# Kernel tuning notes

Measured on AMD Instinct MI355X. Metric: run time of the kernel, lower is better.

Reference implementation:

```python
import jax, jax.numpy as jnp
import numpy as np

DT = 0.001
TAU_MEM = 0.02
TAU_SYN = 0.005
THRESHOLD = 1.0


def conv2d(x, w, b, stride, pad):
    # x: [N,C,H,W], w: [O,I,kh,kw]
    y = jax.lax.conv_general_dilated(
        x, w, window_strides=(stride, stride),
        padding=[(pad, pad), (pad, pad)],
        dimension_numbers=("NCHW", "OIHW", "NCHW"))
    return y + b[None, :, None, None]


def lif_scan(current_t_first):
    # current_t_first: [T, B, C, H, W]; LIF with reset='subtract'
    alpha = jnp.exp(jnp.asarray(-DT / TAU_MEM, dtype=current_t_first.dtype))
    beta = jnp.exp(jnp.asarray(-DT / TAU_SYN, dtype=current_t_first.dtype))
    state_shape = current_t_first.shape[1:]
    init = (jnp.zeros(state_shape, current_t_first.dtype),
            jnp.zeros(state_shape, current_t_first.dtype))

    def step(carry, i_t):
        syn, mem = carry
        syn = beta * syn + i_t
        mem = alpha * mem + syn
        spike = (mem >= THRESHOLD).astype(i_t.dtype)
        mem = mem - THRESHOLD * spike  # subtract reset
        return (syn, mem), spike

    _, spikes = jax.lax.scan(step, init, current_t_first)
    return spikes  # [T, B, C, H, W]


def spiking_conv(x, w, b, stride, pad):
    # x: [B, C, H, W, T] -> spikes [B, O, H', W', T]
    B, C, H, W, T = x.shape
    xt = jnp.moveaxis(x, -1, 0)                 # [T,B,C,H,W]
    y = conv2d(xt.reshape(T * B, C, H, W), w, b, stride, pad)
    y = y.reshape(T, B, *y.shape[1:])           # [T,B,O,H',W']
    spikes = lif_scan(y)
    return jnp.moveaxis(spikes, 0, -1)          # [B,O,H',W',T]


def setup_inputs() -> dict:
    key = jax.random.key(0)
    ks = jax.random.split(key, 9)
    B, H, W, T = 4, 128, 128, 10
    num_classes = 80
    det_ch = (num_classes + 5) * 3  # 255

    def init_w(k, shape):
        fan_in = shape[1] * shape[2] * shape[3]
        bound = 1.0 / np.sqrt(fan_in)
        return jax.random.uniform(k, shape, jnp.float32, -bound, bound)

    x = jax.random.uniform(ks[0], (B, 2, H, W, T), jnp.float32)
    return {
        "x": x,
        "w1": init_w(ks[1], (64, 2, 3, 3)),   "b1": jax.random.uniform(ks[2], (64,), jnp.float32, -0.2, 0.2),
        "w2": init_w(ks[3], (128, 64, 3, 3)), "b2": jax.random.uniform(ks[4], (128,), jnp.float32, -0.04, 0.04),
        "w3": init_w(ks[5], (256, 128, 3, 3)),"b3": jax.random.uniform(ks[6], (256,), jnp.float32, -0.03, 0.03),
        "wd": init_w(ks[7], (det_ch, 256, 1, 1)), "bd": jax.random.uniform(ks[8], (det_ch,), jnp.float32, -0.06, 0.06),
    }


def reference(x, w1, b1, w2, b2, w3, b3, wd, bd):
    h = spiking_conv(x, w1, b1, stride=1, pad=1)   # [B,64,128,128,T]
    h = spiking_conv(h, w2, b2, stride=2, pad=1)   # [B,128,64,64,T]
    h = spiking_conv(h, w3, b3, stride=2, pad=1)   # [B,256,32,32,T]
    h_pooled = jnp.mean(h, axis=-1)                # mean over time
    detections = conv2d(h_pooled, wd, bd, stride=1, pad=0)  # [B,255,32,32]
    return detections
```

## Files before the change

kernel.cpp:

```cpp
#include <hip/hip_runtime.h>
#include <stdint.h>
#include <string.h>
#include <cmath>


#define BB 4
#define TT 10

typedef short bf16x8 __attribute__((ext_vector_type(8)));
typedef float f32x4  __attribute__((ext_vector_type(4)));

#define MFMA16(a, b, c) __builtin_amdgcn_mfma_f32_16x16x32_bf16((a), (b), (c), 0, 0, 0)


__global__ __launch_bounds__(256) void zpad1v(uint32_t* __restrict__ buf) {
    uint32_t* p = buf + (size_t)blockIdx.x * 544896u;
    for (int i = threadIdx.x; i < 8320; i += 256) {
        if (i < 4224) p[i] = 0u;
        else {
            int j = i - 4224;
            int row = 1 + (j >> 5), cih = (j >> 4) & 1, e = j & 15;
            p[row * 4224 + 2112 + cih * 1056 + e] = 0u;
        }
    }
}

__global__ __launch_bounds__(256) void zpad3v(uint32_t* __restrict__ buf) {
    uint32_t* p = buf + (size_t)blockIdx.x * 282880u;
    for (int i = threadIdx.x; i < 8448; i += 256) {
        if (i < 4352) p[i] = 0u;
        else {
            int j = i - 4352;
            int row = 1 + (j >> 6), cih = (j >> 4) & 3, e = j & 15;
            p[row * 4352 + 2176 + cih * 544 + e] = 0u;
        }
    }
}

__global__ __launch_bounds__(256) void conv1_lif(
    const float* __restrict__ x,
    const float* __restrict__ w1,
    const float* __restrict__ b1,
    unsigned short* __restrict__ s1p2,
    float alpha, float beta)
{
    __shared__ float xs[2][3][10][10];
    __shared__ float wsh[18][64];
    __shared__ uint32_t spk[40][68];
    const int tid = threadIdx.x;
    const int b = blockIdx.z, h = blockIdx.y, w0 = blockIdx.x * 8;

    for (int i = tid; i < 1152; i += 256) {
        int co = i & 63, tap = i >> 6;
        wsh[tap][co] = w1[co * 18 + tap];
    }
    for (int i = tid; i < 600; i += 256) {
        int t = i % 10; int rest = i / 10;
        int wi = rest % 10; rest /= 10;
        int kh = rest % 3; int ci = rest / 3;
        int hh = h - 1 + kh, ww = w0 - 1 + wi;
        float v = 0.f;
        if (hh >= 0 && hh < 128 && ww >= 0 && ww < 128)
            v = x[(((b * 2 + ci) * 128 + hh) * 128 + ww) * 10 + t];
        xs[ci][kh][wi][t] = v;
    }
    __syncthreads();

    const int px  = tid & 7;
    const int cog = (tid >> 3) * 2;
    float acc[2][10];
#pragma unroll
    for (int c = 0; c < 2; ++c)
#pragma unroll
        for (int t = 0; t < 10; ++t) acc[c][t] = 0.f;

#pragma unroll
    for (int tap = 0; tap < 18; ++tap) {
        const int ci = tap / 9, kh = (tap % 9) / 3, kw = tap % 3;
        float2 wv = *(const float2*)&wsh[tap][cog];
#pragma unroll
        for (int t = 0; t < 10; ++t) {
            float xv = xs[ci][kh][px + kw][t];
            acc[0][t] = __fmaf_rn(wv.x, xv, acc[0][t]);
            acc[1][t] = __fmaf_rn(wv.y, xv, acc[1][t]);
        }
    }
    const int pr    = px & 1;
    const int col2l = px >> 1;
    const int comb0 = pr * 2 + (cog >> 5);
    const int ipos  = col2l * 16 + ((cog & 31) >> 1);
    const float bv0 = b1[cog], bv1 = b1[cog + 1];
    float syn0 = 0.f, mem0 = 0.f, syn1 = 0.f, mem1 = 0.f;
#pragma unroll
    for (int t = 0; t < 10; ++t) {
        float cur0 = __fadd_rn(acc[0][t], bv0);
        syn0 = __fadd_rn(__fmul_rn(beta, syn0), cur0);
        mem0 = __fadd_rn(__fmul_rn(alpha, mem0), syn0);
        bool s0 = (mem0 >= 1.0f);
        mem0 = __fsub_rn(mem0, s0 ? 1.0f : 0.0f);
        float cur1 = __fadd_rn(acc[1][t], bv1);
        syn1 = __fadd_rn(__fmul_rn(beta, syn1), cur1);
        mem1 = __fadd_rn(__fmul_rn(alpha, mem1), syn1);
        bool s1 = (mem1 >= 1.0f);
        mem1 = __fsub_rn(mem1, s1 ? 1.0f : 0.0f);
        spk[t * 4 + comb0][ipos] =
            (s0 ? 0x3F80u : 0u) | ((s1 ? 0x3F80u : 0u) << 16);
    }
    __syncthreads();

    uint32_t* sg = (uint32_t*)s1p2;
    const int e = tid & 63;
#pragma unroll
    for (int k = 0; k < 10; ++k) {
        const int combo = k * 4 + (tid >> 6);
        const int t  = combo >> 2;
        const int pp = (combo >> 1) & 1;
        const int ch = combo & 1;
        const uint32_t ga = (uint32_t)(t * BB + b) * 544896u
            + ((uint32_t)((h + 1) * 8448 + pp * 4224 + ch * 2112
                          + ((w0 >> 1) + pp) * 32) >> 1) + e;
        sg[ga] = spk[combo][e];
    }
}

__global__ __launch_bounds__(256) void wtrans2c(
    const float* __restrict__ w2, unsigned short* __restrict__ wtb)
{
    int i = blockIdx.x * 256 + threadIdx.x;
    if (i >= 73728) return;
    int co  = i / 576;
    int rem = i - co * 576;
    int ci  = rem / 9;
    int tap = rem - ci * 9;
    float w = w2[i];
    uint32_t uw  = __float_as_uint(w);
    uint32_t h16 = (uw + 0x7FFFu + ((uw >> 16) & 1u)) >> 16;
    float hf = __uint_as_float(h16 << 16);
    float r1 = w - hf;
    uint32_t ur1 = __float_as_uint(r1);
    uint32_t m16 = (ur1 + 0x7FFFu + ((ur1 >> 16) & 1u)) >> 16;
    float mf = __uint_as_float(m16 << 16);
    float r2 = r1 - mf;
    uint32_t ur2 = __float_as_uint(r2);
    uint32_t l16 = (ur2 + 0x7FFFu + ((ur2 >> 16) & 1u)) >> 16;

    int cobi = co >> 6, coL = co & 63;
    int wid = coL >> 4, l15 = coL & 15;
    int c = ci >> 5, r5 = ci & 31;
    int g = r5 >> 3, e = r5 & 7;
    size_t base = (size_t)(cobi * 27 + tap * 3) * 4096
                + (size_t)(((wid * 2 + c) * 64 + (g * 16 + l15)) * 8 + e);
    wtb[base]        = (unsigned short)h16;
    wtb[base + 4096] = (unsigned short)m16;
    wtb[base + 8192] = (unsigned short)l16;
}

__global__ __launch_bounds__(256) void wtrans3c(
    const float* __restrict__ w3, unsigned short* __restrict__ wtb)
{
    int i = blockIdx.x * 256 + threadIdx.x;
    if (i >= 294912) return;
    int co  = i / 1152;
    int rem = i - co * 1152;
    int ci  = rem / 9;
    int tap = rem - ci * 9;
    float w = w3[i];
    uint32_t uw  = __float_as_uint(w);
    uint32_t h16 = (uw + 0x7FFFu + ((uw >> 16) & 1u)) >> 16;
    float hf = __uint_as_float(h16 << 16);
    float r1 = w - hf;
    uint32_t ur1 = __float_as_uint(r1);
    uint32_t m16 = (ur1 + 0x7FFFu + ((ur1 >> 16) & 1u)) >> 16;
    float mf = __uint_as_float(m16 << 16);
    float r2 = r1 - mf;
    uint32_t ur2 = __float_as_uint(r2);
    uint32_t l16 = (ur2 + 0x7FFFu + ((ur2 >> 16) & 1u)) >> 16;

    int cobi = co >> 6, coL = co & 63;
    int wq = coL >> 4, l15 = coL & 15;
    int cc = ci >> 5, r5 = ci & 31;
    int g = r5 >> 3, e = r5 & 7;
    size_t base = (size_t)(cobi * 27 + tap * 3) * 8192
                + (size_t)(((wq * 4 + cc) * 64 + (g * 16 + l15)) * 8 + e);
    wtb[base]         = (unsigned short)h16;
    wtb[base + 8192]  = (unsigned short)m16;
    wtb[base + 16384] = (unsigned short)l16;
}

#define VMCNT(n) do { __builtin_amdgcn_sched_barrier(0); \
    asm volatile("s_waitcnt vmcnt(" #n ")" ::: "memory"); \
    __builtin_amdgcn_sched_barrier(0); } while (0)
#define SB() __builtin_amdgcn_sched_barrier(0)
#define BARR() do { __builtin_amdgcn_sched_barrier(0); \
    __builtin_amdgcn_s_barrier(); \
    __builtin_amdgcn_sched_barrier(0); } while (0)
#define PRIO1() __builtin_amdgcn_s_setprio(1)
#define PRIO0() __builtin_amdgcn_s_setprio(0)

__global__ __launch_bounds__(512) void conv2_mfma(
    const unsigned short* __restrict__ s1p2,
    const unsigned short* __restrict__ wtb,
    float* __restrict__ p2)
{
    __shared__ alignas(16) unsigned short Bs[3][4096];
    const int tid  = threadIdx.x;
    const int lane = tid & 63, w = tid >> 6;
    const int r = lane & 15, g = lane >> 4;
    const int f = blockIdx.z;
    const int hb = blockIdx.x;

    const unsigned short* fb = s1p2 + (uint32_t)f * 1089792u;
    const unsigned short* wB = wtb + (uint32_t)(w >> 2) * (27u * 4096u)
                             + (uint32_t)(w & 3) * 1024u + (uint32_t)lane * 8u;
    const uint32_t lfo = (uint32_t)(r * 32 + g * 8);

    f32x4 acc[4];
#pragma unroll
    for (int mt = 0; mt < 4; ++mt) acc[mt] = (f32x4){0.f, 0.f, 0.f, 0.f};
    bf16x8 bA[6], bB[6];

#define STAGE2(tap_, slot_) do { \
    const int kh_ = (tap_) / 3, kw_ = (tap_) % 3; \
    const int p_ = (kw_ == 1) ? 0 : 1; \
    const int cf_ = (kw_ == 2) ? 1 : 0; \
    const int mt_ = w >> 1, c_ = w & 1; \
    const unsigned short* src_ = fb + (uint32_t)(2 * hb + kh_) * 8448u \
        + (uint32_t)p_ * 4224u + (uint32_t)c_ * 2112u \
        + (uint32_t)(mt_ * 16 + cf_) * 32u + lfo; \
    __builtin_amdgcn_global_load_lds( \
        (const __attribute__((address_space(1))) unsigned int*)(const void*)src_, \
        (__attribute__((address_space(3))) unsigned int*)(void*)(&Bs[slot_][w * 512]), \
        16, 0, 0); \
} while (0)

#define LOADB2(tap_, DST) do { _Pragma("unroll") \
    for (int t_ = 0; t_ < 3; ++t_) { _Pragma("unroll") \
        for (int c_ = 0; c_ < 2; ++c_) \
            DST[t_ * 2 + c_] = *(const bf16x8*)(wB + (uint32_t)((tap_) * 3 + t_) * 4096u + c_ * 512u); \
    } } while (0)

#define COMP2(slot_, BU) do { \
    bf16x8 af_[8]; \
    _Pragma("unroll") \
    for (int q_ = 0; q_ < 8; ++q_) \
        af_[q_] = *(const bf16x8*)&Bs[slot_][q_ * 512 + lane * 8]; \
    _Pragma("unroll") \
    for (int t_ = 0; t_ < 3; ++t_) { _Pragma("unroll") \
        for (int c_ = 0; c_ < 2; ++c_) { \
            bf16x8 b_ = BU[t_ * 2 + c_]; \
            acc[0] = MFMA16(b_, af_[0 + c_], acc[0]); \
            acc[1] = MFMA16(b_, af_[2 + c_], acc[1]); \
            acc[2] = MFMA16(b_, af_[4 + c_], acc[2]); \
            acc[3] = MFMA16(b_, af_[6 + c_], acc[3]); \
        } } } while (0)

#define PH2(tap_, snxt_, scur_, BU, BN) do { \
    SB(); STAGE2((tap_) + 1, snxt_); LOADB2((tap_) + 1, BN); SB(); \
    VMCNT(7); BARR(); \
    PRIO1(); COMP2(scur_, BU); PRIO0(); SB(); \
} while (0)

    STAGE2(0, 0); LOADB2(0, bA);
    PH2(0, 1, 0, bA, bB); PH2(1, 2, 1, bB, bA); PH2(2, 0, 2, bA, bB);
    PH2(3, 1, 0, bB, bA); PH2(4, 2, 1, bA, bB); PH2(5, 0, 2, bB, bA);
    PH2(6, 1, 0, bA, bB); PH2(7, 2, 1, bB, bA);
    SB(); VMCNT(0); BARR();
    PRIO1(); COMP2(2, bA); PRIO0();

#pragma unroll
    for (int mt = 0; mt < 4; ++mt)
        *(f32x4*)&p2[((uint32_t)f * 4096u + hb * 64 + mt * 16 + r) * 128u
                     + w * 16 + g * 4] = acc[mt];
#undef STAGE2
#undef LOADB2
#undef COMP2
#undef PH2
}

__global__ __launch_bounds__(256) void lif_s2_t(
    const float* __restrict__ pa, const float* __restrict__ bias,
    unsigned short* __restrict__ s2p3, float alpha, float beta)
{
    const int tid = threadIdx.x;
    const int b   = blockIdx.z;
    const int px  = blockIdx.x * 8 + (tid >> 5);
    const int co0 = (tid & 31) * 4;
    const int h = px >> 6, w = px & 63;
    float4 bv = *(const float4*)&bias[co0];
    const float bva[4] = {bv.x, bv.y, bv.z, bv.w};
    float syn[4] = {0.f,0.f,0.f,0.f}, mem[4] = {0.f,0.f,0.f,0.f};
    const int pr = w & 1;
    const int col2 = (w + pr) >> 1;
    unsigned short* sp = s2p3 + (uint32_t)(h + 1) * 8704u + pr * 4352u
                       + (co0 >> 5) * 1088u + col2 * 32u + (co0 & 31);
    for (int t = 0; t < TT; ++t) {
        const int f = t * BB + b;
        const uint32_t idx = ((uint32_t)f * 4096u + px) * 128u + co0;
        float4 A = *(const float4*)&pa[idx];
        const float va[4] = {A.x, A.y, A.z, A.w};
        uint32_t pk[2] = {0u, 0u};
#pragma unroll
        for (int j = 0; j < 4; ++j) {
            float c = __fadd_rn(va[j], bva[j]);
            syn[j] = __fadd_rn(__fmul_rn(beta, syn[j]), c);
            mem[j] = __fadd_rn(__fmul_rn(alpha, mem[j]), syn[j]);
            bool sc = (mem[j] >= 1.0f);
            mem[j] = __fsub_rn(mem[j], sc ? 1.0f : 0.0f);
            pk[j >> 1] |= (sc ? 0x3F80u : 0u) << ((j & 1) * 16);
        }
        *(uint2*)(sp + (uint32_t)f * 565760u) = make_uint2(pk[0], pk[1]);
    }
}

__global__ __launch_bounds__(512) void conv3_mfma3(
    const unsigned short* __restrict__ s2p3,
    const unsigned short* __restrict__ wtb,
    float* __restrict__ p3)
{
    __shared__ alignas(16) unsigned short Bs[3][4096];
    const int tid  = threadIdx.x;
    const int lane = tid & 63, w = tid >> 6;
    const int r = lane & 15, g = lane >> 4;
    const int f = blockIdx.z, cb2 = blockIdx.y;
    const int h0 = blockIdx.x * 2;

    const unsigned short* fb = s2p3 + (uint32_t)f * 565760u;
    const unsigned short* wB = wtb + (uint32_t)(cb2 * 2 + (w >> 2)) * (27u * 8192u)
                             + (uint32_t)(w & 3) * 2048u + (uint32_t)lane * 8u;
    const uint32_t lfo = (uint32_t)(r * 32 + g * 8);

    f32x4 acc[4];
#pragma unroll
    for (int mt = 0; mt < 4; ++mt) acc[mt] = (f32x4){0.f, 0.f, 0.f, 0.f};
    bf16x8 bA[6], bB[6];

#define STAGE3(tap_, half_, slot_) do { \
    const int kh_ = (tap_) / 3, kw_ = (tap_) % 3; \
    const int p_ = (kw_ == 1) ? 0 : 1; \
    const int cf_ = (kw_ == 2) ? 1 : 0; \
    const int mt_ = w >> 1, j_ = w & 1; \
    const unsigned short* src_ = fb \
        + (uint32_t)(2 * (h0 + (mt_ >> 1)) + kh_) * 8704u \
        + (uint32_t)p_ * 4352u + (uint32_t)((half_) * 2 + j_) * 1088u \
        + (uint32_t)((mt_ & 1) * 16 + cf_) * 32u + lfo; \
    __builtin_amdgcn_global_load_lds( \
        (const __attribute__((address_space(1))) unsigned int*)(const void*)src_, \
        (__attribute__((address_space(3))) unsigned int*)(void*)(&Bs[slot_][w * 512]), \
        16, 0, 0); \
} while (0)

#define LOADB3(tap_, half_, DST) do { _Pragma("unroll") \
    for (int t_ = 0; t_ < 3; ++t_) { _Pragma("unroll") \
        for (int j_ = 0; j_ < 2; ++j_) \
            DST[t_ * 2 + j_] = *(const bf16x8*)(wB + (uint32_t)((tap_) * 3 + t_) * 8192u \
                + (uint32_t)((half_) * 2 + j_) * 512u); \
    } } while (0)

#define COMP3(slot_, BU) do { \
    bf16x8 af_[8]; \
    _Pragma("unroll") \
    for (int q_ = 0; q_ < 8; ++q_) \
        af_[q_] = *(const bf16x8*)&Bs[slot_][q_ * 512 + lane * 8]; \
    _Pragma("unroll") \
    for (int t_ = 0; t_ < 3; ++t_) { _Pragma("unroll") \
        for (int j_ = 0; j_ < 2; ++j_) { \
            bf16x8 b_ = BU[t_ * 2 + j_]; \
            acc[0] = MFMA16(af_[0 + j_], b_, acc[0]); \
            acc[1] = MFMA16(af_[2 + j_], b_, acc[1]); \
            acc[2] = MFMA16(af_[4 + j_], b_, acc[2]); \
            acc[3] = MFMA16(af_[6 + j_], b_, acc[3]); \
        } } } while (0)

#define PH3(ntap_, nhalf_, snxt_, scur_, BU, BN) do { \
    SB(); STAGE3(ntap_, nhalf_, snxt_); LOADB3(ntap_, nhalf_, BN); SB(); \
    VMCNT(7); BARR(); \
    PRIO1(); COMP3(scur_, BU); PRIO0(); SB(); \
} while (0)

    STAGE3(0, 0, 0); LOADB3(0, 0, bA);
    PH3(0, 1, 1, 0, bA, bB); PH3(1, 0, 2, 1, bB, bA); PH3(1, 1, 0, 2, bA, bB);
    PH3(2, 0, 1, 0, bB, bA); PH3(2, 1, 2, 1, bA, bB); PH3(3, 0, 0, 2, bB, bA);
    PH3(3, 1, 1, 0, bA, bB); PH3(4, 0, 2, 1, bB, bA); PH3(4, 1, 0, 2, bA, bB);
    PH3(5, 0, 1, 0, bB, bA); PH3(5, 1, 2, 1, bA, bB); PH3(6, 0, 0, 2, bB, bA);
    PH3(6, 1, 1, 0, bA, bB); PH3(7, 0, 2, 1, bB, bA); PH3(7, 1, 0, 2, bA, bB);
    PH3(8, 0, 1, 0, bB, bA); PH3(8, 1, 2, 1, bA, bB);
    SB(); VMCNT(0); BARR();
    PRIO1(); COMP3(2, bB); PRIO0();

#pragma unroll
    for (int mt = 0; mt < 4; ++mt) {
        const int hh = h0 + (mt >> 1);
        const int wc = (mt & 1) * 16 + g * 4;
        *(f32x4*)&p3[((uint32_t)(f * 256 + cb2 * 128 + w * 16 + r) * 32u + hh) * 32u + wc] = acc[mt];
    }
#undef STAGE3
#undef LOADB3
#undef COMP3
#undef PH3
}

__global__ __launch_bounds__(256) void lif_mean1(
    const float* __restrict__ p3, const float* __restrict__ bias,
    float* __restrict__ pooled, float alpha, float beta)
{
    const int px = (blockIdx.x * 256 + threadIdx.x) * 4;
    const int co = blockIdx.y;
    const int b  = blockIdx.z;
    const float bv = bias[co];
    float syn[4] = {0.f,0.f,0.f,0.f}, mem[4] = {0.f,0.f,0.f,0.f};
    float sum[4] = {0.f,0.f,0.f,0.f};
    for (int t = 0; t < TT; ++t) {
        const int idx = ((t * BB + b) * 256 + co) * 1024 + px;
        float4 a = *(const float4*)&p3[idx];
        const float va[4] = {a.x, a.y, a.z, a.w};
#pragma unroll
        for (int j = 0; j < 4; ++j) {
            float cu = __fadd_rn(va[j], bv);
            syn[j] = __fadd_rn(__fmul_rn(beta, syn[j]), cu);
            mem[j] = __fadd_rn(__fmul_rn(alpha, mem[j]), syn[j]);
            bool sc = (mem[j] >= 1.0f);
            float sp = sc ? 1.0f : 0.0f;
            mem[j] = __fsub_rn(mem[j], sp);
            sum[j] = __fadd_rn(sum[j], sp);
        }
    }
    *(float4*)&pooled[(b * 256 + co) * 1024 + px] =
        make_float4(sum[0] / 10.0f, sum[1] / 10.0f, sum[2] / 10.0f, sum[3] / 10.0f);
}

__global__ __launch_bounds__(256) void det_conv(
    const float* __restrict__ pooled,
    const float* __restrict__ wd,
    const float* __restrict__ bd,
    float* __restrict__ out)
{
    __shared__ float wtl[16][64];
    __shared__ float ps[16][64];
    const int tid = threadIdx.x;
    const int b = blockIdx.z;
    const int o_base = blockIdx.y * 64;
    const int px_base = blockIdx.x * 64;
    const int o_off = (tid >> 4) * 4;
    const int px_off = (tid & 15) * 4;
    float acc[4][4];
#pragma unroll
    for (int c = 0; c < 4; ++c) {
        int o = o_base + o_off + c;
        float bv = (o < 255) ? bd[o] : 0.f;
#pragma unroll
        for (int j = 0; j < 4; ++j) acc[c][j] = bv;
    }
    for (int cc = 0; cc < 16; ++cc) {
        for (int k = tid; k < 1024; k += 256) {
            int o = k & 63, ci = k >> 6;
            wtl[ci][o] = (o_base + o < 255) ? wd[(o_base + o) * 256 + cc * 16 + ci] : 0.f;
            ps[ci][o] = pooled[(b * 256 + cc * 16 + ci) * 1024 + px_base + o];
        }
        __syncthreads();
#pragma unroll
        for (int ci = 0; ci < 16; ++ci) {
            float4 wv = *(const float4*)&wtl[ci][o_off];
            float4 sv = *(const float4*)&ps[ci][px_off];
            acc[0][0] += wv.x * sv.x; acc[0][1] += wv.x * sv.y;
            acc[0][2] += wv.x * sv.z; acc[0][3] += wv.x * sv.w;
            acc[1][0] += wv.y * sv.x; acc[1][1] += wv.y * sv.y;
            acc[1][2] += wv.y * sv.z; acc[1][3] += wv.y * sv.w;
            acc[2][0] += wv.z * sv.x; acc[2][1] += wv.z * sv.y;
            acc[2][2] += wv.z * sv.z; acc[2][3] += wv.z * sv.w;
            acc[3][0] += wv.w * sv.x; acc[3][1] += wv.w * sv.y;
            acc[3][2] += wv.w * sv.z; acc[3][3] += wv.w * sv.w;
        }
        __syncthreads();
    }
#pragma unroll
    for (int c = 0; c < 4; ++c) {
        int o = o_base + o_off + c;
        if (o < 255)
            *(float4*)&out[(b * 255 + o) * 1024 + px_base + px_off] =
                make_float4(acc[c][0], acc[c][1], acc[c][2], acc[c][3]);
    }
}

extern "C" void kernel_launch(void* const* d_in, const int* in_sizes, int n_in,
                              void* d_out, int out_size, void* d_ws, size_t ws_size,
                              hipStream_t stream) {
    const float* x  = (const float*)d_in[0];
    const float* w1 = (const float*)d_in[1];
    const float* b1 = (const float*)d_in[2];
    const float* w2 = (const float*)d_in[3];
    const float* b2 = (const float*)d_in[4];
    const float* w3 = (const float*)d_in[5];
    const float* b3 = (const float*)d_in[6];
    const float* wd = (const float*)d_in[7];
    const float* bd = (const float*)d_in[8];
    float* out = (float*)d_out;

    uint8_t* wsb = (uint8_t*)d_ws;
    unsigned short* s1p2 = (unsigned short*)(wsb + 256);
    float*   p3     = (float*)(wsb + 256);
    float*   p2     = (float*)(wsb + 87183616u);
    float*   pooled = (float*)(wsb + 87183616u);
    unsigned short* s2p3 = (unsigned short*)(wsb + 171069696u);
    unsigned short* wt2b = (unsigned short*)(wsb + 216330496u);
    unsigned short* wt3b = (unsigned short*)(wsb + 216772864u);

    float alpha, beta;
    { uint32_t ab = 0x3F7383C6u; memcpy(&alpha, &ab, 4); }
    { uint32_t bb = 0x3F519857u; memcpy(&beta,  &bb, 4); }

    zpad1v<<<40, 256, 0, stream>>>((uint32_t*)s1p2);
    zpad3v<<<40, 256, 0, stream>>>((uint32_t*)s2p3);
    wtrans2c<<<288, 256, 0, stream>>>(w2, wt2b);
    wtrans3c<<<1152, 256, 0, stream>>>(w3, wt3b);
    conv1_lif<<<dim3(16, 128, 4), 256, 0, stream>>>(x, w1, b1, s1p2, alpha, beta);
    conv2_mfma<<<dim3(64, 1, 40), 512, 0, stream>>>(s1p2, wt2b, p2);
    lif_s2_t<<<dim3(512, 1, 4), 256, 0, stream>>>(p2, b2, s2p3, alpha, beta);
    conv3_mfma3<<<dim3(16, 2, 40), 512, 0, stream>>>(s2p3, wt3b, p3);
    lif_mean1<<<dim3(1, 256, 4), 256, 0, stream>>>(p3, b3, pooled, alpha, beta);
    det_conv<<<dim3(16, 4, 4), 256, 0, stream>>>(pooled, wd, bd, out);
}
```

Measured before the change: 302.7 us.

## Split conv2/conv3 MFMA blocks into 256-thread blocks over output-channel halves

Each conv block now has 4 waves instead of 8. The output channels are split across an extra grid dimension, so each block covers 64 output channels and each wave stages two LDS chunks instead of one. This doubles the block count, which should give the scheduler more blocks and smaller barrier groups. In exchange, every activation tile is loaded twice (once per channel half), adding global and L2 traffic, and the vmcnt wait is adjusted to match the extra load.

```diff
diff --git a/kernel.cpp b/kernel.cpp
--- a/kernel.cpp
+++ b/kernel.cpp
@@ -197,7 +197,7 @@
 #define PRIO1() __builtin_amdgcn_s_setprio(1)
 #define PRIO0() __builtin_amdgcn_s_setprio(0)
 
-__global__ __launch_bounds__(512) void conv2_mfma(
+__global__ __launch_bounds__(256) void conv2_mfma(
     const unsigned short* __restrict__ s1p2,
     const unsigned short* __restrict__ wtb,
     float* __restrict__ p2)
@@ -207,11 +207,12 @@
     const int lane = tid & 63, w = tid >> 6;
     const int r = lane & 15, g = lane >> 4;
     const int f = blockIdx.z;
+    const int cobi = blockIdx.y;
     const int hb = blockIdx.x;
 
     const unsigned short* fb = s1p2 + (uint32_t)f * 1089792u;
-    const unsigned short* wB = wtb + (uint32_t)(w >> 2) * (27u * 4096u)
-                             + (uint32_t)(w & 3) * 1024u + (uint32_t)lane * 8u;
+    const unsigned short* wB = wtb + (uint32_t)cobi * (27u * 4096u)
+                             + (uint32_t)w * 1024u + (uint32_t)lane * 8u;
     const uint32_t lfo = (uint32_t)(r * 32 + g * 8);
 
     f32x4 acc[4];
@@ -223,15 +224,16 @@
     const int kh_ = (tap_) / 3, kw_ = (tap_) % 3; \
     const int p_ = (kw_ == 1) ? 0 : 1; \
     const int cf_ = (kw_ == 2) ? 1 : 0; \
-    const int mt_ = w >> 1, c_ = w & 1; \
-    const unsigned short* src_ = fb + (uint32_t)(2 * hb + kh_) * 8448u \
-        + (uint32_t)p_ * 4224u + (uint32_t)c_ * 2112u \
-        + (uint32_t)(mt_ * 16 + cf_) * 32u + lfo; \
-    __builtin_amdgcn_global_load_lds( \
-        (const __attribute__((address_space(1))) unsigned int*)(const void*)src_, \
-        (__attribute__((address_space(3))) unsigned int*)(void*)(&Bs[slot_][w * 512]), \
-        16, 0, 0); \
-} while (0)
+    _Pragma("unroll") \
+    for (int c_ = 0; c_ < 2; ++c_) { \
+        const unsigned short* src_ = fb + (uint32_t)(2 * hb + kh_) * 8448u \
+            + (uint32_t)p_ * 4224u + (uint32_t)c_ * 2112u \
+            + (uint32_t)(w * 16 + cf_) * 32u + lfo; \
+        __builtin_amdgcn_global_load_lds( \
+            (const __attribute__((address_space(1))) unsigned int*)(const void*)src_, \
+            (__attribute__((address_space(3))) unsigned int*)(void*)(&Bs[slot_][(w * 2 + c_) * 512]), \
+            16, 0, 0); \
+    } } while (0)
 
 #define LOADB2(tap_, DST) do { _Pragma("unroll") \
     for (int t_ = 0; t_ < 3; ++t_) { _Pragma("unroll") \
@@ -256,7 +258,7 @@
 
 #define PH2(tap_, snxt_, scur_, BU, BN) do { \
     SB(); STAGE2((tap_) + 1, snxt_); LOADB2((tap_) + 1, BN); SB(); \
-    VMCNT(7); BARR(); \
+    VMCNT(8); BARR(); \
     PRIO1(); COMP2(scur_, BU); PRIO0(); SB(); \
 } while (0)
 
@@ -270,7 +272,7 @@
 #pragma unroll
     for (int mt = 0; mt < 4; ++mt)
         *(f32x4*)&p2[((uint32_t)f * 4096u + hb * 64 + mt * 16 + r) * 128u
-                     + w * 16 + g * 4] = acc[mt];
+                     + cobi * 64 + w * 16 + g * 4] = acc[mt];
 #undef STAGE2
 #undef LOADB2
 #undef COMP2
@@ -312,7 +314,7 @@
     }
 }
 
-__global__ __launch_bounds__(512) void conv3_mfma3(
+__global__ __launch_bounds__(256) void conv3_mfma3(
     const unsigned short* __restrict__ s2p3,
     const unsigned short* __restrict__ wtb,
     float* __restrict__ p3)
@@ -321,12 +323,13 @@
     const int tid  = threadIdx.x;
     const int lane = tid & 63, w = tid >> 6;
     const int r = lane & 15, g = lane >> 4;
-    const int f = blockIdx.z, cb2 = blockIdx.y;
+    const int f = blockIdx.z;
+    const int cobi = blockIdx.y;
     const int h0 = blockIdx.x * 2;
 
     const unsigned short* fb = s2p3 + (uint32_t)f * 565760u;
-    const unsigned short* wB = wtb + (uint32_t)(cb2 * 2 + (w >> 2)) * (27u * 8192u)
-                             + (uint32_t)(w & 3) * 2048u + (uint32_t)lane * 8u;
+    const unsigned short* wB = wtb + (uint32_t)cobi * (27u * 8192u)
+                             + (uint32_t)w * 2048u + (uint32_t)lane * 8u;
     const uint32_t lfo = (uint32_t)(r * 32 + g * 8);
 
     f32x4 acc[4];
@@ -338,16 +341,17 @@
     const int kh_ = (tap_) / 3, kw_ = (tap_) % 3; \
     const int p_ = (kw_ == 1) ? 0 : 1; \
     const int cf_ = (kw_ == 2) ? 1 : 0; \
-    const int mt_ = w >> 1, j_ = w & 1; \
-    const unsigned short* src_ = fb \
-        + (uint32_t)(2 * (h0 + (mt_ >> 1)) + kh_) * 8704u \
-        + (uint32_t)p_ * 4352u + (uint32_t)((half_) * 2 + j_) * 1088u \
-        + (uint32_t)((mt_ & 1) * 16 + cf_) * 32u + lfo; \
-    __builtin_amdgcn_global_load_lds( \
-        (const __attribute__((address_space(1))) unsigned int*)(const void*)src_, \
-        (__attribute__((address_space(3))) unsigned int*)(void*)(&Bs[slot_][w * 512]), \
-        16, 0, 0); \
-} while (0)
+    _Pragma("unroll") \
+    for (int j_ = 0; j_ < 2; ++j_) { \
+        const unsigned short* src_ = fb \
+            + (uint32_t)(2 * (h0 + (w >> 1)) + kh_) * 8704u \
+            + (uint32_t)p_ * 4352u + (uint32_t)((half_) * 2 + j_) * 1088u \
+            + (uint32_t)((w & 1) * 16 + cf_) * 32u + lfo; \
+        __builtin_amdgcn_global_load_lds( \
+            (const __attribute__((address_space(1))) unsigned int*)(const void*)src_, \
+            (__attribute__((address_space(3))) unsigned int*)(void*)(&Bs[slot_][(w * 2 + j_) * 512]), \
+            16, 0, 0); \
+    } } while (0)
 
 #define LOADB3(tap_, half_, DST) do { _Pragma("unroll") \
     for (int t_ = 0; t_ < 3; ++t_) { _Pragma("unroll") \
@@ -373,7 +377,7 @@
 
 #define PH3(ntap_, nhalf_, snxt_, scur_, BU, BN) do { \
     SB(); STAGE3(ntap_, nhalf_, snxt_); LOADB3(ntap_, nhalf_, BN); SB(); \
-    VMCNT(7); BARR(); \
+    VMCNT(8); BARR(); \
     PRIO1(); COMP3(scur_, BU); PRIO0(); SB(); \
 } while (0)
 
@@ -391,7 +395,7 @@
     for (int mt = 0; mt < 4; ++mt) {
         const int hh = h0 + (mt >> 1);
         const int wc = (mt & 1) * 16 + g * 4;
-        *(f32x4*)&p3[((uint32_t)(f * 256 + cb2 * 128 + w * 16 + r) * 32u + hh) * 32u + wc] = acc[mt];
+        *(f32x4*)&p3[((uint32_t)(f * 256 + cobi * 64 + w * 16 + r) * 32u + hh) * 32u + wc] = acc[mt];
     }
 #undef STAGE3
 #undef LOADB3
@@ -513,9 +517,9 @@
     wtrans2c<<<288, 256, 0, stream>>>(w2, wt2b);
     wtrans3c<<<1152, 256, 0, stream>>>(w3, wt3b);
     conv1_lif<<<dim3(16, 128, 4), 256, 0, stream>>>(x, w1, b1, s1p2, alpha, beta);
-    conv2_mfma<<<dim3(64, 1, 40), 512, 0, stream>>>(s1p2, wt2b, p2);
+    conv2_mfma<<<dim3(64, 2, 40), 256, 0, stream>>>(s1p2, wt2b, p2);
     lif_s2_t<<<dim3(512, 1, 4), 256, 0, stream>>>(p2, b2, s2p3, alpha, beta);
-    conv3_mfma3<<<dim3(16, 2, 40), 512, 0, stream>>>(s2p3, wt3b, p3);
+    conv3_mfma3<<<dim3(16, 4, 40), 256, 0, stream>>>(s2p3, wt3b, p3);
     lif_mean1<<<dim3(1, 256, 4), 256, 0, stream>>>(p3, b3, pooled, alpha, beta);
     det_conv<<<dim3(16, 4, 4), 256, 0, stream>>>(pooled, wd, bd, out);
 }
```

New measurement: 310.3 us. 2.5% more time.
